# Performance work log

Hardware: AMD Instinct MI355X
Metric: run time of the kernel (lower is better)

The kernel has to match this reference:

```python
import jax, jax.numpy as jnp
import numpy as np

SDF_THRESHOLD = 5e-05
N_STEPS = 256
ROOTFIND_ITERS = 8  # ceil(log2(((6-2)/255) / (2*5e-5))) -> exact torch iteration count


def sdf_fn(p, W1, b1, W2, b2, W3, b3):
    # neural SDF: unit sphere + small MLP perturbation; p is [..., 3] -> [...]
    base = jnp.linalg.norm(p, axis=-1) - 1.0
    h = jnp.tanh(p @ W1 + b1)
    h = jnp.tanh(h @ W2 + b2)
    return base + 0.05 * (h @ W3 + b3)[..., 0]


def setup_inputs() -> dict:
    key = jax.random.key(0)
    ks = jax.random.split(key, 6)
    N, H = 8192, 64
    ray_o = jnp.array([0.0, 0.0, 4.0]) + 0.1 * jax.random.normal(ks[0], (N, 3))
    target = 0.5 * jax.random.normal(ks[1], (N, 3))  # aim near the unit sphere
    d = target - ray_o
    ray_d = d / jnp.linalg.norm(d, axis=-1, keepdims=True)
    min_dis = jnp.full((N,), 2.0, jnp.float32)
    max_dis = jnp.full((N,), 6.0, jnp.float32)
    min_dis_outer = jnp.full((N,), 1.5, jnp.float32)
    max_dis_outer = jnp.full((N,), 6.5, jnp.float32)
    work_mask = jnp.ones((N,), bool)
    floor_dist = jnp.full((N, 1), 5.0, jnp.float32)
    W1 = jax.random.normal(ks[2], (3, H)) / np.sqrt(3.0)
    W2 = jax.random.normal(ks[3], (H, H)) / np.sqrt(H)
    W3 = jax.random.normal(ks[4], (H, 1)) / np.sqrt(H)
    b1 = jnp.zeros((H,)); b2 = jnp.zeros((H,)); b3 = jnp.zeros((1,))
    return {"ray_o": ray_o, "ray_d": ray_d, "min_dis": min_dis, "max_dis": max_dis,
            "min_dis_outer": min_dis_outer, "max_dis_outer": max_dis_outer,
            "work_mask": work_mask, "floor_dist": floor_dist,
            "W1": W1, "b1": b1, "W2": W2, "b2": b2, "W3": W3, "b3": b3}


def _ray_trace(ray_o, ray_d, min_dis, max_dis, min_dis_outer, max_dis_outer,
               work_mask, floor_dist, W1, b1, W2, b2, W3, b3):
    params = (W1, b1, W2, b2, W3, b3)
    sdf = lambda p: sdf_fn(p, *params)
    thr = SDF_THRESHOLD

    # ---- sphere tracing (sphere_tracing_iters=0: loop body never runs) ----
    acc0 = min_dis_outer                                  # [N]
    pts0 = ray_o + ray_d * acc0[:, None]                  # [N,3]
    sdf0 = sdf(pts0)                                      # [N]
    unfinished = work_mask & (jnp.abs(sdf0) > thr) & (acc0 < max_dis_outer)
    conv = work_mask & ~unfinished & (jnp.abs(sdf0) <= thr) & (acc0 < max_dis_outer)

    # ---- dense ray sampling (computed for all rays, merged via `unfinished`) ----
    t = jnp.linspace(0.0, 1.0, N_STEPS)
    dis = min_dis[:, None] + t[None, :] * (max_dis - min_dis)[:, None]   # [N,S]
    pts = ray_o[:, None, :] + ray_d[:, None, :] * dis[..., None]         # [N,S,3]
    sv = sdf(pts.reshape(-1, 3)).reshape(dis.shape)                      # [N,S]
    amin = jnp.argmin(jnp.abs(sv), axis=-1)                              # [N]
    s_pts = jnp.take_along_axis(pts, amin[:, None, None], axis=1)[:, 0]
    s_sdf = jnp.take_along_axis(sv, amin[:, None], axis=1)[:, 0]
    s_dis = jnp.take_along_axis(dis, amin[:, None], axis=1)[:, 0]

    # first sign transition: min of sign(sdf) * [S..1]
    w = jnp.arange(N_STEPS, 0, -1, dtype=sv.dtype)
    tmp = jnp.sign(sv) * w
    min_val = jnp.min(tmp, axis=-1)
    min_idx = jnp.argmin(tmp, axis=-1)
    rf_mask = (min_val < 0.0) & (min_idx >= 1)
    idx = jnp.maximum(min_idx, 1)  # safe gather; masked out where rf_mask is False
    z_low = jnp.take_along_axis(dis, (idx - 1)[:, None], axis=1)[:, 0]
    z_high = jnp.take_along_axis(dis, idx[:, None], axis=1)[:, 0]

    # ---- bisection rootfind: exactly ROOTFIND_ITERS global iterations ----
    def body(carry, _):
        dl, dh = carry
        dm = 0.5 * (dl + dh)
        fm = sdf(ray_o + ray_d * dm[:, None])
        pos = fm > 0
        return (jnp.where(pos, dm, dl), jnp.where(pos, dh, dm)), None

    (d_low, d_high), _ = jax.lax.scan(body, (z_low, z_high), None, length=ROOTFIND_ITERS)
    d_mid = 0.5 * (d_low + d_high)
    p_mid = ray_o + ray_d * d_mid[:, None]
    f_mid = sdf(p_mid)
    s_pts = jnp.where(rf_mask[:, None], p_mid, s_pts)
    s_sdf = jnp.where(rf_mask, f_mid, s_sdf)
    s_dis = jnp.where(rf_mask, d_mid, s_dis)

    # ---- merge sampler results into sphere-tracing results ----
    conv = jnp.where(unfinished, rf_mask, conv)
    points = jnp.where(unfinished[:, None], s_pts, pts0)
    sdf_out = jnp.where(unfinished, s_sdf, sdf0)
    dist = jnp.where(unfinished, s_dis, acc0)

    real_mask = conv
    real_points = points

    # ---- mock floor: fill background rays with floor intersection ----
    floor_pts = ray_o + ray_d * floor_dist  # [N,3]
    bg = ~conv
    points = jnp.where(bg[:, None], floor_pts, points)
    sdf_out = jnp.where(bg, jnp.zeros_like(sdf_out), sdf_out)
    dist = jnp.where(bg, floor_dist[:, 0], dist)
    conv = conv | bg  # all True after mock floor
    return conv, real_mask, points, real_points, sdf_out, dist


def reference(ray_o, ray_d, min_dis, max_dis, min_dis_outer, max_dis_outer,
              work_mask, floor_dist, W1, b1, W2, b2, W3, b3):
    return _ray_trace(ray_o, ray_d, min_dis, max_dis, min_dis_outer, max_dis_outer,
                      work_mask, floor_dist, W1, b1, W2, b2, W3, b3)
```

## Files before the change

kernel.cpp:

```cpp
#include <hip/hip_runtime.h>
#include <math.h>


#define NSTEPS 256
#define H 64
#define SDF_THR 5e-5f
#define RF_ITERS 8
#define C2LN 2.8853900817779268f

typedef __attribute__((ext_vector_type(8))) short bf16x8;
typedef __attribute__((ext_vector_type(4))) float f32x4;

union FragU { unsigned int u[4]; bf16x8 v; };

__device__ __forceinline__ float step_t(int s) {
    float t = (float)s * (1.0f / 255.0f);
    if (s == NSTEPS - 1) t = 1.0f;
    return t;
}
__device__ __forceinline__ float tanh_pre(float y) {
    const float t = __builtin_amdgcn_exp2f(y);
    return fmaf(-2.0f, __builtin_amdgcn_rcpf(t + 1.0f), 1.0f);
}
__device__ __forceinline__ float tanh_fast(float x) {
    const float t = __builtin_amdgcn_exp2f(x * C2LN);
    return fmaf(-2.0f, __builtin_amdgcn_rcpf(t + 1.0f), 1.0f);
}
__device__ __forceinline__ float sgprf(float v) {
    return __uint_as_float(__builtin_amdgcn_readfirstlane(__float_as_uint(v)));
}
__device__ __forceinline__ float dpp_row_sum16(float x) {
    float t;
    t = __uint_as_float(__builtin_amdgcn_update_dpp(0, __float_as_uint(x), 0x111, 0xF, 0xF, true)); x += t;
    t = __uint_as_float(__builtin_amdgcn_update_dpp(0, __float_as_uint(x), 0x112, 0xF, 0xF, true)); x += t;
    t = __uint_as_float(__builtin_amdgcn_update_dpp(0, __float_as_uint(x), 0x114, 0xF, 0xF, true)); x += t;
    t = __uint_as_float(__builtin_amdgcn_update_dpp(0, __float_as_uint(x), 0x118, 0xF, 0xF, true)); x += t;
    return x;
}

__global__ __launch_bounds__(256, 3) void raytrace_kernel(
    const float* __restrict__ ray_o, const float* __restrict__ ray_d,
    const float* __restrict__ min_dis, const float* __restrict__ max_dis,
    const float* __restrict__ min_dis_outer, const float* __restrict__ max_dis_outer,
    const float* __restrict__ floor_dist,
    const float* __restrict__ W1, const float* __restrict__ b1,
    const float* __restrict__ W2, const float* __restrict__ b2,
    const float* __restrict__ W3, const float* __restrict__ b3,
    float* __restrict__ out, int N)
{
    __shared__ __align__(16) unsigned char bfrag[16 * 1024];
    __shared__ float4 abLDS[4][32];
    __shared__ float sv_lds[4][256];
    __shared__ float h1bc[4][64];

    const int tid  = (int)threadIdx.x;
    const int lane = tid & 63;
    const int wid  = tid >> 6;
    const int wave = ((int)blockIdx.x << 2) | wid;
    const int r    = (wave < N) ? wave : (N - 1);

    const float ox = sgprf(ray_o[r * 3 + 0]), oy = sgprf(ray_o[r * 3 + 1]), oz = sgprf(ray_o[r * 3 + 2]);
    const float dx = sgprf(ray_d[r * 3 + 0]), dy = sgprf(ray_d[r * 3 + 1]), dz = sgprf(ray_d[r * 3 + 2]);
    const float mind = sgprf(min_dis[r]);
    const float range = sgprf(max_dis[r] - min_dis[r]);
    const float mindo = sgprf(min_dis_outer[r]), maxdo = sgprf(max_dis_outer[r]);
    const float floord = sgprf(floor_dist[r]);
    const float b3s = sgprf(b3[0]);

    {
        const int fg = tid >> 6;
        #pragma unroll
        for (int q = 0; q < 4; ++q) {
            const int f  = q * 4 + fg;
            const int kt = f >> 3, nt = (f >> 1) & 3, sp = f & 1;
            const int n  = nt * 16 + (lane & 15);
            const int kb = kt * 32 + (lane >> 4) * 8;
            unsigned int up[4];
            #pragma unroll
            for (int e2 = 0; e2 < 4; ++e2) {
                const float w0 = W2[(kb + 2 * e2    ) * H + n] * C2LN;
                const float w1 = W2[(kb + 2 * e2 + 1) * H + n] * C2LN;
                unsigned hb0 = __float_as_uint(w0) & 0xFFFF0000u;
                unsigned hb1 = __float_as_uint(w1) & 0xFFFF0000u;
                if (sp) {
                    hb0 = __float_as_uint(w0 - __uint_as_float(hb0)) & 0xFFFF0000u;
                    hb1 = __float_as_uint(w1 - __uint_as_float(hb1)) & 0xFFFF0000u;
                }
                up[e2] = (hb0 >> 16) | hb1;
            }
            *(uint4*)&bfrag[f * 1024 + lane * 16] = make_uint4(up[0], up[1], up[2], up[3]);
        }
    }
    {
        const float w1x = W1[lane], w1y = W1[64 + lane], w1z = W1[128 + lane];
        const float Ai = fmaf(oz, w1z, fmaf(oy, w1y, fmaf(ox, w1x, b1[lane]))) * C2LN;
        const float Bi = fmaf(dz, w1z, fmaf(dy, w1y, dx * w1x)) * C2LN;
        ((float2*)&abLDS[wid][0])[lane] = make_float2(Ai, Bi);
    }
    __syncthreads();
    if (wave >= N) return;

    bf16x8 Breg[16];
    #pragma unroll
    for (int f = 0; f < 16; ++f) {
        Breg[f] = *(const bf16x8*)&bfrag[f * 1024 + lane * 16];
        asm volatile("" : "+v"(Breg[f]));
    }
    f32x4 abr[8];
    #pragma unroll
    for (int kt = 0; kt < 2; ++kt)
        #pragma unroll
        for (int e2 = 0; e2 < 4; ++e2) {
            abr[kt * 4 + e2] = *(const f32x4*)&abLDS[wid][kt * 16 + (lane >> 4) * 4 + e2];
            asm volatile("" : "+v"(abr[kt * 4 + e2]));
        }

    const float b2r0 = b2[ 0 + (lane & 15)] * C2LN, b2r1 = b2[16 + (lane & 15)] * C2LN;
    const float b2r2 = b2[32 + (lane & 15)] * C2LN, b2r3 = b2[48 + (lane & 15)] * C2LN;
    const float w3r0 = W3[ 0 + (lane & 15)], w3r1 = W3[16 + (lane & 15)];
    const float w3r2 = W3[32 + (lane & 15)], w3r3 = W3[48 + (lane & 15)];

    #pragma unroll 1
    for (int T = 0; T < 16; ++T) {
        const int sA = T * 16 + (lane & 15);
        const float disA = fmaf(step_t(sA), range, mind);
        FragU ahi[2];
        #pragma unroll
        for (int kt = 0; kt < 2; ++kt) {
            #pragma unroll
            for (int e2 = 0; e2 < 4; ++e2) {
                const f32x4 qv = abr[kt * 4 + e2];
                const float v0 = tanh_pre(fmaf(disA, qv.y, qv.x));
                const float v1 = tanh_pre(fmaf(disA, qv.w, qv.z));
                unsigned pk;
                asm("v_cvt_pk_bf16_f32 %0, %1, %2" : "=v"(pk) : "v"(v0), "v"(v1));
                ahi[kt].u[e2] = pk;
            }
        }
        f32x4 C0 = {b2r0, b2r0, b2r0, b2r0};
        f32x4 C1 = {b2r1, b2r1, b2r1, b2r1};
        f32x4 C2 = {b2r2, b2r2, b2r2, b2r2};
        f32x4 C3 = {b2r3, b2r3, b2r3, b2r3};
        #pragma unroll
        for (int kt = 0; kt < 2; ++kt) {
            const bf16x8 ah = ahi[kt].v;
#define MM(Cn, nt) { \
    Cn = __builtin_amdgcn_mfma_f32_16x16x32_bf16(ah, Breg[(kt * 4 + (nt)) * 2 + 0], Cn, 0, 0, 0); \
    Cn = __builtin_amdgcn_mfma_f32_16x16x32_bf16(ah, Breg[(kt * 4 + (nt)) * 2 + 1], Cn, 0, 0, 0); }
            MM(C0, 0) MM(C1, 1) MM(C2, 2) MM(C3, 3)
#undef MM
        }
        #pragma unroll
        for (int rr = 0; rr < 4; ++rr) {
            float o3r = tanh_pre(C0[rr]) * w3r0;
            o3r = fmaf(tanh_pre(C1[rr]), w3r1, o3r);
            o3r = fmaf(tanh_pre(C2[rr]), w3r2, o3r);
            o3r = fmaf(tanh_pre(C3[rr]), w3r3, o3r);
            o3r = dpp_row_sum16(o3r);
            if ((lane & 15) == 15)
                sv_lds[wid][rr * 64 + T * 4 + (lane >> 4)] = o3r;
        }
    }

    float track_abs = INFINITY; int track_idx = 0; float track_sv = 0.0f;
    float track_tmp = INFINITY; int track_tidx = 0;
    #pragma unroll
    for (int q = 0; q < 4; ++q) {
        const float o3 = sv_lds[wid][q * 64 + lane];
        const int s = lane * 4 + q;
        const float dis = fmaf(step_t(s), range, mind);
        const float px = fmaf(dx, dis, ox);
        const float py = fmaf(dy, dis, oy);
        const float pz = fmaf(dz, dis, oz);
        const float base = sqrtf(fmaf(px, px, fmaf(py, py, pz * pz))) - 1.0f;
        const float sv = fmaf(0.05f, o3 + b3s, base);
        const float asv = fabsf(sv);
        if (asv < track_abs) { track_abs = asv; track_idx = s; track_sv = sv; }
        const float sgn = (sv > 0.0f) ? 1.0f : ((sv < 0.0f) ? -1.0f : 0.0f);
        const float tmp = sgn * (float)(NSTEPS - s);
        if (tmp < track_tmp) { track_tmp = tmp; track_tidx = s; }
    }
    #pragma unroll
    for (int off = 32; off; off >>= 1) {
        float o_abs = __shfl_xor(track_abs, off);
        int   o_idx = __shfl_xor(track_idx, off);
        float o_sv  = __shfl_xor(track_sv, off);
        if (o_abs < track_abs || (o_abs == track_abs && o_idx < track_idx)) {
            track_abs = o_abs; track_idx = o_idx; track_sv = o_sv;
        }
        float o_tmp = __shfl_xor(track_tmp, off);
        int   o_tix = __shfl_xor(track_tidx, off);
        if (o_tmp < track_tmp || (o_tmp == track_tmp && o_tix < track_tidx)) {
            track_tmp = o_tmp; track_tidx = o_tix;
        }
    }

    const float w1c0 = W1[0 * H + lane];
    const float w1c1 = W1[1 * H + lane];
    const float w1c2 = W1[2 * H + lane];
    const float b1c = b1[lane], b2c = b2[lane], w3c = W3[lane];
    float w2col[H];
    #pragma unroll
    for (int i = 0; i < H; ++i) w2col[i] = W2[i * H + lane];

    auto eval_sdf = [&](float dist) -> float {
        const float px = fmaf(dx, dist, ox);
        const float py = fmaf(dy, dist, oy);
        const float pz = fmaf(dz, dist, oz);
        const float h1v = tanh_fast(fmaf(pz, w1c2, fmaf(py, w1c1, fmaf(px, w1c0, b1c))));
        h1bc[wid][lane] = h1v;
        __threadfence_block();
        float a0 = 0.0f, a1 = 0.0f, a2 = 0.0f, a3 = 0.0f;
        const float4* hp = (const float4*)&h1bc[wid][0];
        #pragma unroll
        for (int t4 = 0; t4 < 16; ++t4) {
            const float4 h4 = hp[t4];
            a0 = fmaf(h4.x, w2col[4 * t4 + 0], a0);
            a1 = fmaf(h4.y, w2col[4 * t4 + 1], a1);
            a2 = fmaf(h4.z, w2col[4 * t4 + 2], a2);
            a3 = fmaf(h4.w, w2col[4 * t4 + 3], a3);
        }
        const float acc = b2c + ((a0 + a1) + (a2 + a3));
        float part = tanh_fast(acc) * w3c;
        #pragma unroll
        for (int off = 32; off; off >>= 1) part += __shfl_xor(part, off);
        const float base = sqrtf(fmaf(px, px, fmaf(py, py, pz * pz))) - 1.0f;
        return fmaf(0.05f, part + b3s, base);
    };

    const float acc0 = mindo;
    const float sdf0 = eval_sdf(acc0);
    const bool unfinished = (fabsf(sdf0) > SDF_THR) && (acc0 < maxdo);
    bool conv = (!unfinished) && (fabsf(sdf0) <= SDF_THR) && (acc0 < maxdo);

    const bool rf_mask = (track_tmp < 0.0f) && (track_tidx >= 1);
    const int idx = (track_tidx > 1) ? track_tidx : 1;
    float dl = fmaf(step_t(idx - 1), range, mind);
    float dh = fmaf(step_t(idx), range, mind);

    #pragma unroll 1
    for (int it = 0; it < RF_ITERS; ++it) {
        const float dm = 0.5f * (dl + dh);
        const float fm = eval_sdf(dm);
        if (fm > 0.0f) dl = dm; else dh = dm;
    }
    const float d_mid = 0.5f * (dl + dh);
    const float f_mid = eval_sdf(d_mid);

    float s_dis = fmaf(step_t(track_idx), range, mind);
    float s_sdf = track_sv;
    if (rf_mask) { s_dis = d_mid; s_sdf = f_mid; }
    const float spx = fmaf(dx, s_dis, ox), spy = fmaf(dy, s_dis, oy), spz = fmaf(dz, s_dis, oz);

    if (unfinished) conv = rf_mask;
    float Px, Py, Pz, SD, DI;
    if (unfinished) { Px = spx; Py = spy; Pz = spz; SD = s_sdf; DI = s_dis; }
    else {
        Px = fmaf(dx, acc0, ox); Py = fmaf(dy, acc0, oy); Pz = fmaf(dz, acc0, oz);
        SD = sdf0; DI = acc0;
    }

    const bool real_mask = conv;
    const float RPx = Px, RPy = Py, RPz = Pz;

    if (!conv) {
        Px = fmaf(dx, floord, ox); Py = fmaf(dy, floord, oy); Pz = fmaf(dz, floord, oz);
        SD = 0.0f; DI = floord;
    }

    if (lane == 0) {
        const size_t n = (size_t)N;
        out[r] = 1.0f;
        out[n + r] = real_mask ? 1.0f : 0.0f;
        out[2 * n + (size_t)r * 3 + 0] = Px;
        out[2 * n + (size_t)r * 3 + 1] = Py;
        out[2 * n + (size_t)r * 3 + 2] = Pz;
        out[5 * n + (size_t)r * 3 + 0] = RPx;
        out[5 * n + (size_t)r * 3 + 1] = RPy;
        out[5 * n + (size_t)r * 3 + 2] = RPz;
        out[8 * n + r] = SD;
        out[9 * n + r] = DI;
    }
}

extern "C" void kernel_launch(void* const* d_in, const int* in_sizes, int n_in,
                              void* d_out, int out_size, void* d_ws, size_t ws_size,
                              hipStream_t stream) {
    const float* ray_o         = (const float*)d_in[0];
    const float* ray_d         = (const float*)d_in[1];
    const float* min_dis       = (const float*)d_in[2];
    const float* max_dis       = (const float*)d_in[3];
    const float* min_dis_outer = (const float*)d_in[4];
    const float* max_dis_outer = (const float*)d_in[5];
    const float* floor_dist    = (const float*)d_in[7];
    const float* W1 = (const float*)d_in[8];
    const float* b1 = (const float*)d_in[9];
    const float* W2 = (const float*)d_in[10];
    const float* b2 = (const float*)d_in[11];
    const float* W3 = (const float*)d_in[12];
    const float* b3 = (const float*)d_in[13];

    const int N = in_sizes[2];
    const int threads = 256;
    const int blocks = (N * 64 + threads - 1) / threads;

    raytrace_kernel<<<blocks, threads, 0, stream>>>(
        ray_o, ray_d, min_dis, max_dis, min_dis_outer, max_dis_outer, floor_dist,
        W1, b1, W2, b2, W3, b3, (float*)d_out, N);
}
```

Baseline: 99.01 us.

## Replace sequential bisection with two 16-point MFMA batched interval searches

Replaces the 8 sequential scalar bisection SDF evaluations, plus the separate initial-point evaluation, with two batched 16-sample evaluations done on the bf16 MFMA path. Each batch brackets the sign change among 16 subintervals, giving the same total refinement as 8 halvings in two dependent rounds instead of nine. The start-point SDF is folded into slot 0 of the first tile. This cuts serial latency, but the bisection decisions now use bf16 hidden activations, so the chosen interval can differ from the fp32 reference near the root.

```diff
diff --git a/kernel.cpp b/kernel.cpp
--- a/kernel.cpp
+++ b/kernel.cpp
@@ -5,7 +5,6 @@
 #define NSTEPS 256
 #define H 64
 #define SDF_THR 5e-5f
-#define RF_ITERS 8
 #define C2LN 2.8853900817779268f
 
 typedef __attribute__((ext_vector_type(8))) short bf16x8;
@@ -195,6 +194,89 @@
         }
     }
 
+    auto tile_eval = [&](float d0, float bb, float stp) {
+        const int slot = lane & 15;
+        const float disA = (slot == 0) ? d0 : fmaf((float)slot, stp, bb);
+        FragU ahi[2];
+        #pragma unroll
+        for (int kt = 0; kt < 2; ++kt) {
+            #pragma unroll
+            for (int e2 = 0; e2 < 4; ++e2) {
+                const f32x4 qv = abr[kt * 4 + e2];
+                const float v0 = tanh_pre(fmaf(disA, qv.y, qv.x));
+                const float v1 = tanh_pre(fmaf(disA, qv.w, qv.z));
+                unsigned pk;
+                asm("v_cvt_pk_bf16_f32 %0, %1, %2" : "=v"(pk) : "v"(v0), "v"(v1));
+                ahi[kt].u[e2] = pk;
+            }
+        }
+        f32x4 C0 = {b2r0, b2r0, b2r0, b2r0};
+        f32x4 C1 = {b2r1, b2r1, b2r1, b2r1};
+        f32x4 C2 = {b2r2, b2r2, b2r2, b2r2};
+        f32x4 C3 = {b2r3, b2r3, b2r3, b2r3};
+        #pragma unroll
+        for (int kt = 0; kt < 2; ++kt) {
+            const bf16x8 ah = ahi[kt].v;
+#define MM(Cn, nt) { \
+    Cn = __builtin_amdgcn_mfma_f32_16x16x32_bf16(ah, Breg[(kt * 4 + (nt)) * 2 + 0], Cn, 0, 0, 0); \
+    Cn = __builtin_amdgcn_mfma_f32_16x16x32_bf16(ah, Breg[(kt * 4 + (nt)) * 2 + 1], Cn, 0, 0, 0); }
+            MM(C0, 0) MM(C1, 1) MM(C2, 2) MM(C3, 3)
+#undef MM
+        }
+        #pragma unroll
+        for (int rr = 0; rr < 4; ++rr) {
+            float o3r = tanh_pre(C0[rr]) * w3r0;
+            o3r = fmaf(tanh_pre(C1[rr]), w3r1, o3r);
+            o3r = fmaf(tanh_pre(C2[rr]), w3r2, o3r);
+            o3r = fmaf(tanh_pre(C3[rr]), w3r3, o3r);
+            o3r = dpp_row_sum16(o3r);
+            if ((lane & 15) == 15) {
+                const int s = ((lane >> 4) << 2) + rr;
+                const float ds = (s == 0) ? d0 : fmaf((float)s, stp, bb);
+                const float px = fmaf(dx, ds, ox);
+                const float py = fmaf(dy, ds, oy);
+                const float pz = fmaf(dz, ds, oz);
+                const float base = sqrtf(fmaf(px, px, fmaf(py, py, pz * pz))) - 1.0f;
+                sv_lds[wid][s] = fmaf(0.05f, o3r + b3s, base);
+            }
+        }
+        __threadfence_block();
+    };
+
+    const bool rf_mask = (track_tmp < 0.0f) && (track_tidx >= 1);
+    const int idx = (track_tidx > 1) ? track_tidx : 1;
+    const float dl = fmaf(step_t(idx - 1), range, mind);
+    const float dh = fmaf(step_t(idx), range, mind);
+
+    const float w16a = (dh - dl) * 0.0625f;
+    tile_eval(mindo, dl, w16a);
+    const float sdf0 = sv_lds[wid][0];
+    int lo = 0, hi = 16;
+    #pragma unroll
+    for (int st = 0; st < 4; ++st) {
+        const int mid = (lo + hi) >> 1;
+        if (sv_lds[wid][mid] > 0.0f) lo = mid; else hi = mid;
+    }
+    const float dl2 = (lo == 0) ? dl : fmaf((float)lo, w16a, dl);
+    const float dh2 = (hi == 16) ? dh : fmaf((float)hi, w16a, dl);
+    __threadfence_block();
+
+    const float w16b = (dh2 - dl2) * 0.0625f;
+    tile_eval(dl2, dl2, w16b);
+    lo = 0; hi = 16;
+    #pragma unroll
+    for (int st = 0; st < 4; ++st) {
+        const int mid = (lo + hi) >> 1;
+        if (sv_lds[wid][mid] > 0.0f) lo = mid; else hi = mid;
+    }
+    const float dl3 = (lo == 0) ? dl2 : fmaf((float)lo, w16b, dl2);
+    const float dh3 = (hi == 16) ? dh2 : fmaf((float)hi, w16b, dl2);
+    const float d_mid = 0.5f * (dl3 + dh3);
+
+    const float acc0 = mindo;
+    const bool unfinished = (fabsf(sdf0) > SDF_THR) && (acc0 < maxdo);
+    bool conv = (!unfinished) && (fabsf(sdf0) <= SDF_THR) && (acc0 < maxdo);
+
     const float w1c0 = W1[0 * H + lane];
     const float w1c1 = W1[1 * H + lane];
     const float w1c2 = W1[2 * H + lane];
@@ -203,10 +285,11 @@
     #pragma unroll
     for (int i = 0; i < H; ++i) w2col[i] = W2[i * H + lane];
 
-    auto eval_sdf = [&](float dist) -> float {
-        const float px = fmaf(dx, dist, ox);
-        const float py = fmaf(dy, dist, oy);
-        const float pz = fmaf(dz, dist, oz);
+    float f_mid;
+    {
+        const float px = fmaf(dx, d_mid, ox);
+        const float py = fmaf(dy, d_mid, oy);
+        const float pz = fmaf(dz, d_mid, oz);
         const float h1v = tanh_fast(fmaf(pz, w1c2, fmaf(py, w1c1, fmaf(px, w1c0, b1c))));
         h1bc[wid][lane] = h1v;
         __threadfence_block();
@@ -225,27 +308,8 @@
         #pragma unroll
         for (int off = 32; off; off >>= 1) part += __shfl_xor(part, off);
         const float base = sqrtf(fmaf(px, px, fmaf(py, py, pz * pz))) - 1.0f;
-        return fmaf(0.05f, part + b3s, base);
-    };
-
-    const float acc0 = mindo;
-    const float sdf0 = eval_sdf(acc0);
-    const bool unfinished = (fabsf(sdf0) > SDF_THR) && (acc0 < maxdo);
-    bool conv = (!unfinished) && (fabsf(sdf0) <= SDF_THR) && (acc0 < maxdo);
-
-    const bool rf_mask = (track_tmp < 0.0f) && (track_tidx >= 1);
-    const int idx = (track_tidx > 1) ? track_tidx : 1;
-    float dl = fmaf(step_t(idx - 1), range, mind);
-    float dh = fmaf(step_t(idx), range, mind);
-
-    #pragma unroll 1
-    for (int it = 0; it < RF_ITERS; ++it) {
-        const float dm = 0.5f * (dl + dh);
-        const float fm = eval_sdf(dm);
-        if (fm > 0.0f) dl = dm; else dh = dm;
-    }
-    const float d_mid = 0.5f * (dl + dh);
-    const float f_mid = eval_sdf(d_mid);
+        f_mid = fmaf(0.05f, part + b3s, base);
+    }
 
     float s_dis = fmaf(step_t(track_idx), range, mind);
     float s_sdf = track_sv;
```

After: 93.91 us. 1.05x faster.

## Replace serial bisection root-find with 16-way MFMA tile evaluations

Applied to the files above, without the earlier changes.

Replaces the 8 serial scalar-FMA SDF evaluations of the bisection (plus the sdf0 and final evaluations) with three MFMA tile evaluations. The first tile evaluates sdf0 and 15 interior points of the bracket; two 16-way subdivisions then narrow the bracket as far as 8 bisection steps would, and a third tile computes f_mid. It also folds the W3 dot product algebraically, computing sum(w3) - 2*sum(w3/(exp+1)), and drops the per-lane W2 column registers and LDS broadcast. The risk is that the subdivision points and endpoints are computed differently from the reference's bisection midpoints (including bf16 precision in the root-find), so results may differ slightly.

```diff
diff --git a/kernel.cpp b/kernel.cpp
--- a/kernel.cpp
+++ b/kernel.cpp
@@ -5,7 +5,6 @@
 #define NSTEPS 256
 #define H 64
 #define SDF_THR 5e-5f
-#define RF_ITERS 8
 #define C2LN 2.8853900817779268f
 
 typedef __attribute__((ext_vector_type(8))) short bf16x8;
@@ -20,10 +19,6 @@
 }
 __device__ __forceinline__ float tanh_pre(float y) {
     const float t = __builtin_amdgcn_exp2f(y);
-    return fmaf(-2.0f, __builtin_amdgcn_rcpf(t + 1.0f), 1.0f);
-}
-__device__ __forceinline__ float tanh_fast(float x) {
-    const float t = __builtin_amdgcn_exp2f(x * C2LN);
     return fmaf(-2.0f, __builtin_amdgcn_rcpf(t + 1.0f), 1.0f);
 }
 __device__ __forceinline__ float sgprf(float v) {
@@ -51,7 +46,6 @@
     __shared__ __align__(16) unsigned char bfrag[16 * 1024];
     __shared__ float4 abLDS[4][32];
     __shared__ float sv_lds[4][256];
-    __shared__ float h1bc[4][64];
 
     const int tid  = (int)threadIdx.x;
     const int lane = tid & 63;
@@ -117,13 +111,14 @@
 
     const float b2r0 = b2[ 0 + (lane & 15)] * C2LN, b2r1 = b2[16 + (lane & 15)] * C2LN;
     const float b2r2 = b2[32 + (lane & 15)] * C2LN, b2r3 = b2[48 + (lane & 15)] * C2LN;
-    const float w3r0 = W3[ 0 + (lane & 15)], w3r1 = W3[16 + (lane & 15)];
-    const float w3r2 = W3[32 + (lane & 15)], w3r3 = W3[48 + (lane & 15)];
-
-    #pragma unroll 1
-    for (int T = 0; T < 16; ++T) {
-        const int sA = T * 16 + (lane & 15);
-        const float disA = fmaf(step_t(sA), range, mind);
+    const float w3a = W3[ 0 + (lane & 15)], w3b = W3[16 + (lane & 15)];
+    const float w3c = W3[32 + (lane & 15)], w3d = W3[48 + (lane & 15)];
+    const float w3sum = (w3a + w3b) + (w3c + w3d);
+    const float m2w0 = -2.0f * w3a, m2w1 = -2.0f * w3b;
+    const float m2w2 = -2.0f * w3c, m2w3 = -2.0f * w3d;
+
+    auto tile_core = [&](auto dfn, auto store) {
+        const float disA = dfn(lane & 15);
         FragU ahi[2];
         #pragma unroll
         for (int kt = 0; kt < 2; ++kt) {
@@ -152,14 +147,21 @@
         }
         #pragma unroll
         for (int rr = 0; rr < 4; ++rr) {
-            float o3r = tanh_pre(C0[rr]) * w3r0;
-            o3r = fmaf(tanh_pre(C1[rr]), w3r1, o3r);
-            o3r = fmaf(tanh_pre(C2[rr]), w3r2, o3r);
-            o3r = fmaf(tanh_pre(C3[rr]), w3r3, o3r);
+            float o3r = fmaf(m2w0, __builtin_amdgcn_rcpf(__builtin_amdgcn_exp2f(C0[rr]) + 1.0f), w3sum);
+            o3r = fmaf(m2w1, __builtin_amdgcn_rcpf(__builtin_amdgcn_exp2f(C1[rr]) + 1.0f), o3r);
+            o3r = fmaf(m2w2, __builtin_amdgcn_rcpf(__builtin_amdgcn_exp2f(C2[rr]) + 1.0f), o3r);
+            o3r = fmaf(m2w3, __builtin_amdgcn_rcpf(__builtin_amdgcn_exp2f(C3[rr]) + 1.0f), o3r);
             o3r = dpp_row_sum16(o3r);
             if ((lane & 15) == 15)
-                sv_lds[wid][rr * 64 + T * 4 + (lane >> 4)] = o3r;
-        }
+                store(((lane >> 4) << 2) + rr, o3r);
+        }
+    };
+
+    #pragma unroll 1
+    for (int T = 0; T < 16; ++T) {
+        tile_core(
+            [&](int slot) { return fmaf(step_t(T * 16 + slot), range, mind); },
+            [&](int s, float o3r) { sv_lds[wid][(s & 3) * 64 + T * 4 + (s >> 2)] = o3r; });
     }
 
     float track_abs = INFINITY; int track_idx = 0; float track_sv = 0.0f;
@@ -195,57 +197,57 @@
         }
     }
 
-    const float w1c0 = W1[0 * H + lane];
-    const float w1c1 = W1[1 * H + lane];
-    const float w1c2 = W1[2 * H + lane];
-    const float b1c = b1[lane], b2c = b2[lane], w3c = W3[lane];
-    float w2col[H];
-    #pragma unroll
-    for (int i = 0; i < H; ++i) w2col[i] = W2[i * H + lane];
-
-    auto eval_sdf = [&](float dist) -> float {
-        const float px = fmaf(dx, dist, ox);
-        const float py = fmaf(dy, dist, oy);
-        const float pz = fmaf(dz, dist, oz);
-        const float h1v = tanh_fast(fmaf(pz, w1c2, fmaf(py, w1c1, fmaf(px, w1c0, b1c))));
-        h1bc[wid][lane] = h1v;
+    auto tile_eval = [&](float d0, float bb, float stp) {
+        tile_core(
+            [&](int slot) { return (slot == 0) ? d0 : fmaf((float)slot, stp, bb); },
+            [&](int s, float o3r) {
+                const float ds = (s == 0) ? d0 : fmaf((float)s, stp, bb);
+                const float px = fmaf(dx, ds, ox);
+                const float py = fmaf(dy, ds, oy);
+                const float pz = fmaf(dz, ds, oz);
+                const float base = sqrtf(fmaf(px, px, fmaf(py, py, pz * pz))) - 1.0f;
+                sv_lds[wid][s] = fmaf(0.05f, o3r + b3s, base);
+            });
         __threadfence_block();
-        float a0 = 0.0f, a1 = 0.0f, a2 = 0.0f, a3 = 0.0f;
-        const float4* hp = (const float4*)&h1bc[wid][0];
-        #pragma unroll
-        for (int t4 = 0; t4 < 16; ++t4) {
-            const float4 h4 = hp[t4];
-            a0 = fmaf(h4.x, w2col[4 * t4 + 0], a0);
-            a1 = fmaf(h4.y, w2col[4 * t4 + 1], a1);
-            a2 = fmaf(h4.z, w2col[4 * t4 + 2], a2);
-            a3 = fmaf(h4.w, w2col[4 * t4 + 3], a3);
-        }
-        const float acc = b2c + ((a0 + a1) + (a2 + a3));
-        float part = tanh_fast(acc) * w3c;
-        #pragma unroll
-        for (int off = 32; off; off >>= 1) part += __shfl_xor(part, off);
-        const float base = sqrtf(fmaf(px, px, fmaf(py, py, pz * pz))) - 1.0f;
-        return fmaf(0.05f, part + b3s, base);
     };
 
+    const bool rf_mask = (track_tmp < 0.0f) && (track_tidx >= 1);
+    const int idx = (track_tidx > 1) ? track_tidx : 1;
+    const float dl = fmaf(step_t(idx - 1), range, mind);
+    const float dh = fmaf(step_t(idx), range, mind);
+
+    const float w16a = (dh - dl) * 0.0625f;
+    tile_eval(mindo, dl, w16a);
+    const float sdf0 = sv_lds[wid][0];
+    int lo = 0, hi = 16;
+    #pragma unroll
+    for (int st = 0; st < 4; ++st) {
+        const int mid = (lo + hi) >> 1;
+        if (sv_lds[wid][mid] > 0.0f) lo = mid; else hi = mid;
+    }
+    const float dl2 = (lo == 0) ? dl : fmaf((float)lo, w16a, dl);
+    const float dh2 = (hi == 16) ? dh : fmaf((float)hi, w16a, dl);
+    __threadfence_block();
+
+    const float w16b = (dh2 - dl2) * 0.0625f;
+    tile_eval(dl2, dl2, w16b);
+    lo = 0; hi = 16;
+    #pragma unroll
+    for (int st = 0; st < 4; ++st) {
+        const int mid = (lo + hi) >> 1;
+        if (sv_lds[wid][mid] > 0.0f) lo = mid; else hi = mid;
+    }
+    const float dl3 = (lo == 0) ? dl2 : fmaf((float)lo, w16b, dl2);
+    const float dh3 = (hi == 16) ? dh2 : fmaf((float)hi, w16b, dl2);
+    const float d_mid = 0.5f * (dl3 + dh3);
+    __threadfence_block();
+
+    tile_eval(d_mid, d_mid, 0.0f);
+    const float f_mid = sv_lds[wid][0];
+
     const float acc0 = mindo;
-    const float sdf0 = eval_sdf(acc0);
     const bool unfinished = (fabsf(sdf0) > SDF_THR) && (acc0 < maxdo);
     bool conv = (!unfinished) && (fabsf(sdf0) <= SDF_THR) && (acc0 < maxdo);
-
-    const bool rf_mask = (track_tmp < 0.0f) && (track_tidx >= 1);
-    const int idx = (track_tidx > 1) ? track_tidx : 1;
-    float dl = fmaf(step_t(idx - 1), range, mind);
-    float dh = fmaf(step_t(idx), range, mind);
-
-    #pragma unroll 1
-    for (int it = 0; it < RF_ITERS; ++it) {
-        const float dm = 0.5f * (dl + dh);
-        const float fm = eval_sdf(dm);
-        if (fm > 0.0f) dl = dm; else dh = dm;
-    }
-    const float d_mid = 0.5f * (dl + dh);
-    const float f_mid = eval_sdf(d_mid);
 
     float s_dis = fmaf(step_t(track_idx), range, mind);
     float s_sdf = track_sv;
```

Measured after the change: 93.25 us. -5.8%, faster.
